# Kernel tuning notes

Measured on AMD Instinct MI355X. Metric: run time of the kernel, lower is better.

The kernel has to match this reference:

```python
import jax, jax.numpy as jnp
import numpy as np


def fwht(x):
    """Unnormalized Fast Walsh-Hadamard transform along axis 0 (Sylvester order).
    Equivalent to H @ x where H is the +/-1 Hadamard matrix. x.shape[0] must be a power of 2."""
    D = x.shape[0]
    orig_shape = x.shape
    x = x.reshape(D, -1)
    h = 1
    while h < D:
        x = x.reshape(D // (2 * h), 2, h, -1)
        a = x[:, 0]
        b = x[:, 1]
        x = jnp.stack([a + b, a - b], axis=1)
        h *= 2
    return x.reshape(orig_shape)


def setup_inputs() -> dict:
    D = 4096
    B = 2048
    key = jax.random.key(0)
    k_x, k_eps, k_rho = jax.random.split(key, 3)
    x = jax.random.normal(k_x, (B, D), dtype=jnp.float32)
    epsilon = jax.random.normal(k_eps, (D,), dtype=jnp.float32)
    s1 = jnp.ones((D,), dtype=jnp.float32) * 0.01
    s2 = jnp.ones((D,), dtype=jnp.float32) * 0.01
    g_mu = jnp.zeros((D,), dtype=jnp.float32)
    # g_rho ~ Uniform(-5, -4) as in the torch init
    g_rho = jax.random.uniform(k_rho, (D,), dtype=jnp.float32, minval=-5.0, maxval=-4.0)
    return {"x": x, "epsilon": epsilon, "s1": s1, "s2": s2, "g_mu": g_mu, "g_rho": g_rho}


def reference(x, epsilon, s1, s2, g_mu, g_rho):
    D = s1.shape[0]
    # g_sigma_sqrt_diagonal = softplus(g_rho); sampled diag g = g_mu + sigma * eps.
    # W = diag(s1) @ H @ diag(g) @ H @ diag(s2); mu and sigma terms are linear in g, so combine.
    g = g_mu + jax.nn.softplus(g_rho) * epsilon
    # HS2 = H * s2 (columns of H scaled by s2) = H @ diag(s2) = fwht(diag(s2)) along axis 0
    HS2 = fwht(jnp.diag(s2))                      # [D, D]
    W = s1[:, None] * fwht(g[:, None] * HS2)      # [D, D]
    # F.linear(x, W) = x @ W^T
    return x @ W.T
```

## Files before the change

kernel.cpp:

```cpp
#include <hip/hip_runtime.h>
#include <math.h>

#define DIM 4096
#define ROWS 2048
#define SB 68

typedef _Float16 half8  __attribute__((ext_vector_type(8)));
typedef _Float16 half4  __attribute__((ext_vector_type(4)));
typedef float    float4e __attribute__((ext_vector_type(4)));

__global__ void g_precompute(const float* __restrict__ eps,
                             const float* __restrict__ g_mu,
                             const float* __restrict__ g_rho,
                             float* __restrict__ g) {
    int i = blockIdx.x * blockDim.x + threadIdx.x;
    g[i] = fmaf(log1pf(expf(g_rho[i])), eps[i], g_mu[i]);
}

__device__ __forceinline__ void hx_stage(const _Float16* __restrict__ img,
                                         int n, int q, const half8 Hf[4][2],
                                         float4e acc[4][4]) {
    half8 B[4][2];
#pragma unroll
    for (int J = 0; J < 4; ++J)
#pragma unroll
        for (int Kt = 0; Kt < 2; ++Kt) {
            const _Float16* p = img + (32 * Kt + 8 * q) * SB + 16 * J + n;
            half8 b;
#pragma unroll
            for (int j = 0; j < 8; ++j) b[j] = p[j * SB];
            B[J][Kt] = b;
        }
#pragma unroll
    for (int I = 0; I < 4; ++I)
#pragma unroll
        for (int J = 0; J < 4; ++J) {
            float4e c = {0.0f, 0.0f, 0.0f, 0.0f};
            c = __builtin_amdgcn_mfma_f32_16x16x32_f16(Hf[I][0], B[J][0], c, 0, 0, 0);
            c = __builtin_amdgcn_mfma_f32_16x16x32_f16(Hf[I][1], B[J][1], c, 0, 0, 0);
            acc[I][J] = c;
        }
}

__device__ __forceinline__ void img_write_T(_Float16* __restrict__ img,
                                            int n, int q, const float4e acc[4][4]) {
#pragma unroll
    for (int I = 0; I < 4; ++I)
#pragma unroll
        for (int J = 0; J < 4; ++J) {
            half4 h;
            h[0] = (_Float16)acc[I][J][0];
            h[1] = (_Float16)acc[I][J][1];
            h[2] = (_Float16)acc[I][J][2];
            h[3] = (_Float16)acc[I][J][3];
            *(half4*)(img + (16 * J + n) * SB + 16 * I + 4 * q) = h;
        }
}

__global__ void __launch_bounds__(256, 2)
whvi_mfma(const float* __restrict__ x, const float* __restrict__ s1,
          const float* __restrict__ s2, const float* __restrict__ g,
          float* __restrict__ out) {
    const int lane = threadIdx.x & 63;
    const int wid  = threadIdx.x >> 6;
    const int row  = blockIdx.x * 4 + wid;
    const int n = lane & 15, q = lane >> 4;

    __shared__ __align__(16) _Float16 lds[4 * 64 * SB];
    _Float16* __restrict__ img = lds + wid * 64 * SB;

    const float4e* __restrict__ xr  = (const float4e*)(x + (size_t)row * DIM);
    const float4e* __restrict__ s2v = (const float4e*)s2;

    float4e xv[16], sv[16];
#pragma unroll
    for (int r = 0; r < 16; ++r) xv[r] = xr[64 * r + lane];
#pragma unroll
    for (int r = 0; r < 16; ++r) sv[r] = s2v[64 * r + lane];

    half8 Hf[4][2];
#pragma unroll
    for (int I = 0; I < 4; ++I)
#pragma unroll
        for (int Kt = 0; Kt < 2; ++Kt) {
            half8 h;
#pragma unroll
            for (int j = 0; j < 8; ++j) {
                int rr = 16 * I + n, cc = 32 * Kt + 8 * q + j;
                h[j] = (__popc(rr & cc) & 1) ? (_Float16)(-1.0f) : (_Float16)(1.0f);
            }
            Hf[I][Kt] = h;
        }

#pragma unroll
    for (int r = 0; r < 16; ++r) {
        float4e p = xv[r] * sv[r];
        half4 h;
        h[0] = (_Float16)p[0]; h[1] = (_Float16)p[1];
        h[2] = (_Float16)p[2]; h[3] = (_Float16)p[3];
        *(half4*)(img + (4 * r + q) * SB + 4 * n) = h;
    }

    float4e acc[4][4];

    hx_stage(img, n, q, Hf, acc);
    img_write_T(img, n, q, acc);
    hx_stage(img, n, q, Hf, acc);

#pragma unroll
    for (int I = 0; I < 4; ++I)
#pragma unroll
        for (int J = 0; J < 4; ++J) {
            const float4e gg = *(const float4e*)(g + 1024 * J + 64 * n + 16 * I + 4 * q);
            acc[I][J] *= gg;
        }

    img_write_T(img, n, q, acc);
    hx_stage(img, n, q, Hf, acc);
    img_write_T(img, n, q, acc);
    hx_stage(img, n, q, Hf, acc);

    float* __restrict__ orow = out + (size_t)row * DIM;
#pragma unroll
    for (int I = 0; I < 4; ++I)
#pragma unroll
        for (int J = 0; J < 4; ++J) {
            const int e = 1024 * J + 64 * n + 16 * I + 4 * q;
            const float4e sg = *(const float4e*)(s1 + e);
            *(float4e*)(orow + e) = acc[I][J] * sg;
        }
}

extern "C" void kernel_launch(void* const* d_in, const int* in_sizes, int n_in,
                              void* d_out, int out_size, void* d_ws, size_t ws_size,
                              hipStream_t stream) {
    const float* x     = (const float*)d_in[0];
    const float* eps   = (const float*)d_in[1];
    const float* s1    = (const float*)d_in[2];
    const float* s2    = (const float*)d_in[3];
    const float* g_mu  = (const float*)d_in[4];
    const float* g_rho = (const float*)d_in[5];
    float* out = (float*)d_out;
    float* g   = (float*)d_ws;

    g_precompute<<<DIM / 256, 256, 0, stream>>>(eps, g_mu, g_rho, g);
    whvi_mfma<<<ROWS / 4, 256, 0, stream>>>(x, s1, s2, g, out);
}
```

Before: 100.2 us.

## Split each row's Hadamard transform across four waves with double-buffered LDS

Each row was handled by a single wave. Now a 256-thread block handles one row, with each wave owning one 16-column slice (J) of the 64x64 image. Stages ping-pong between two LDS buffers, and block-wide barriers separate them. This shrinks per-thread register arrays, so launch bounds can ask for 6 blocks per CU, raising occupancy and the number of blocks for latency hiding. In exchange it adds four __syncthreads per row.

```diff
diff --git a/kernel.cpp b/kernel.cpp
--- a/kernel.cpp
+++ b/kernel.cpp
@@ -18,65 +18,60 @@
 }
 
 __device__ __forceinline__ void hx_stage(const _Float16* __restrict__ img,
-                                         int n, int q, const half8 Hf[4][2],
-                                         float4e acc[4][4]) {
-    half8 B[4][2];
+                                         int n, int q, int J,
+                                         const half8 Hf[4][2], float4e acc[4]) {
+    half8 B[2];
 #pragma unroll
-    for (int J = 0; J < 4; ++J)
+    for (int Kt = 0; Kt < 2; ++Kt) {
+        const _Float16* p = img + (32 * Kt + 8 * q) * SB + 16 * J + n;
+        half8 b;
 #pragma unroll
-        for (int Kt = 0; Kt < 2; ++Kt) {
-            const _Float16* p = img + (32 * Kt + 8 * q) * SB + 16 * J + n;
-            half8 b;
+        for (int j = 0; j < 8; ++j) b[j] = p[j * SB];
+        B[Kt] = b;
+    }
 #pragma unroll
-            for (int j = 0; j < 8; ++j) b[j] = p[j * SB];
-            B[J][Kt] = b;
-        }
-#pragma unroll
-    for (int I = 0; I < 4; ++I)
-#pragma unroll
-        for (int J = 0; J < 4; ++J) {
-            float4e c = {0.0f, 0.0f, 0.0f, 0.0f};
-            c = __builtin_amdgcn_mfma_f32_16x16x32_f16(Hf[I][0], B[J][0], c, 0, 0, 0);
-            c = __builtin_amdgcn_mfma_f32_16x16x32_f16(Hf[I][1], B[J][1], c, 0, 0, 0);
-            acc[I][J] = c;
-        }
+    for (int I = 0; I < 4; ++I) {
+        float4e c = {0.0f, 0.0f, 0.0f, 0.0f};
+        c = __builtin_amdgcn_mfma_f32_16x16x32_f16(Hf[I][0], B[0], c, 0, 0, 0);
+        c = __builtin_amdgcn_mfma_f32_16x16x32_f16(Hf[I][1], B[1], c, 0, 0, 0);
+        acc[I] = c;
+    }
 }
 
 __device__ __forceinline__ void img_write_T(_Float16* __restrict__ img,
-                                            int n, int q, const float4e acc[4][4]) {
+                                            int n, int q, int J,
+                                            const float4e acc[4]) {
 #pragma unroll
-    for (int I = 0; I < 4; ++I)
-#pragma unroll
-        for (int J = 0; J < 4; ++J) {
-            half4 h;
-            h[0] = (_Float16)acc[I][J][0];
-            h[1] = (_Float16)acc[I][J][1];
-            h[2] = (_Float16)acc[I][J][2];
-            h[3] = (_Float16)acc[I][J][3];
-            *(half4*)(img + (16 * J + n) * SB + 16 * I + 4 * q) = h;
-        }
+    for (int I = 0; I < 4; ++I) {
+        half4 h;
+        h[0] = (_Float16)acc[I][0];
+        h[1] = (_Float16)acc[I][1];
+        h[2] = (_Float16)acc[I][2];
+        h[3] = (_Float16)acc[I][3];
+        *(half4*)(img + (16 * J + n) * SB + 16 * I + 4 * q) = h;
+    }
 }
 
-__global__ void __launch_bounds__(256, 2)
+__global__ void __launch_bounds__(256, 6)
 whvi_mfma(const float* __restrict__ x, const float* __restrict__ s1,
           const float* __restrict__ s2, const float* __restrict__ g,
           float* __restrict__ out) {
-    const int lane = threadIdx.x & 63;
-    const int wid  = threadIdx.x >> 6;
-    const int row  = blockIdx.x * 4 + wid;
+    const int tid  = threadIdx.x;
+    const int lane = tid & 63;
+    const int J    = tid >> 6;
+    const int row  = blockIdx.x;
     const int n = lane & 15, q = lane >> 4;
 
-    __shared__ __align__(16) _Float16 lds[4 * 64 * SB];
-    _Float16* __restrict__ img = lds + wid * 64 * SB;
+    __shared__ __align__(16) _Float16 img[2][64 * SB];
 
     const float4e* __restrict__ xr  = (const float4e*)(x + (size_t)row * DIM);
     const float4e* __restrict__ s2v = (const float4e*)s2;
 
-    float4e xv[16], sv[16];
+    float4e xv[4], sv[4];
 #pragma unroll
-    for (int r = 0; r < 16; ++r) xv[r] = xr[64 * r + lane];
+    for (int k = 0; k < 4; ++k) xv[k] = xr[tid + 256 * k];
 #pragma unroll
-    for (int r = 0; r < 16; ++r) sv[r] = s2v[64 * r + lane];
+    for (int k = 0; k < 4; ++k) sv[k] = s2v[tid + 256 * k];
 
     half8 Hf[4][2];
 #pragma unroll
@@ -93,42 +88,44 @@
         }
 
 #pragma unroll
-    for (int r = 0; r < 16; ++r) {
-        float4e p = xv[r] * sv[r];
+    for (int k = 0; k < 4; ++k) {
+        float4e p = xv[k] * sv[k];
         half4 h;
         h[0] = (_Float16)p[0]; h[1] = (_Float16)p[1];
         h[2] = (_Float16)p[2]; h[3] = (_Float16)p[3];
-        *(half4*)(img + (4 * r + q) * SB + 4 * n) = h;
+        *(half4*)(&img[0][(4 * J + 16 * k + q) * SB + 4 * n]) = h;
     }
+    __syncthreads();
 
-    float4e acc[4][4];
+    float4e acc[4];
 
-    hx_stage(img, n, q, Hf, acc);
-    img_write_T(img, n, q, acc);
-    hx_stage(img, n, q, Hf, acc);
+    hx_stage(img[0], n, q, J, Hf, acc);
+    img_write_T(img[1], n, q, J, acc);
+    __syncthreads();
+
+    hx_stage(img[1], n, q, J, Hf, acc);
 
 #pragma unroll
-    for (int I = 0; I < 4; ++I)
-#pragma unroll
-        for (int J = 0; J < 4; ++J) {
-            const float4e gg = *(const float4e*)(g + 1024 * J + 64 * n + 16 * I + 4 * q);
-            acc[I][J] *= gg;
-        }
+    for (int I = 0; I < 4; ++I) {
+        const float4e gg = *(const float4e*)(g + 1024 * J + 64 * n + 16 * I + 4 * q);
+        acc[I] *= gg;
+    }
+    img_write_T(img[0], n, q, J, acc);
+    __syncthreads();
 
-    img_write_T(img, n, q, acc);
-    hx_stage(img, n, q, Hf, acc);
-    img_write_T(img, n, q, acc);
-    hx_stage(img, n, q, Hf, acc);
+    hx_stage(img[0], n, q, J, Hf, acc);
+    img_write_T(img[1], n, q, J, acc);
+    __syncthreads();
+
+    hx_stage(img[1], n, q, J, Hf, acc);
 
     float* __restrict__ orow = out + (size_t)row * DIM;
 #pragma unroll
-    for (int I = 0; I < 4; ++I)
-#pragma unroll
-        for (int J = 0; J < 4; ++J) {
-            const int e = 1024 * J + 64 * n + 16 * I + 4 * q;
-            const float4e sg = *(const float4e*)(s1 + e);
-            *(float4e*)(orow + e) = acc[I][J] * sg;
-        }
+    for (int I = 0; I < 4; ++I) {
+        const int e = 1024 * J + 64 * n + 16 * I + 4 * q;
+        const float4e sg = *(const float4e*)(s1 + e);
+        *(float4e*)(orow + e) = acc[I] * sg;
+    }
 }
 
 extern "C" void kernel_launch(void* const* d_in, const int* in_sizes, int n_in,
@@ -144,5 +141,5 @@
     float* g   = (float*)d_ws;
 
     g_precompute<<<DIM / 256, 256, 0, stream>>>(eps, g_mu, g_rho, g);
-    whvi_mfma<<<ROWS / 4, 256, 0, stream>>>(x, s1, s2, g, out);
+    whvi_mfma<<<ROWS, 256, 0, stream>>>(x, s1, s2, g, out);
 }
```

Measured after the change: 100.8 us. Within noise of the previous version (+0.6%).
